# Kernel tuning notes

Hardware: AMD Instinct MI355X
Metric: run time of the kernel (lower is better)

The kernel has to match this reference:

```python
import jax, jax.numpy as jnp
import numpy as np
from jax import lax

B, T, N = 32, 48, 360   # batch, time steps, ROIs
H = 100                 # LSTM hidden (self.L)
D = 64                  # attention hidden (self.D)
K = 1                   # attention heads (self.K)
NUM_CLASS = 2


def setup_inputs() -> dict:
    key = jax.random.key(0)
    ks = jax.random.split(key, 14)
    s = 0.02
    return {
        "x": jax.random.normal(ks[0], (B, T, N, N), dtype=jnp.float32),
        # GCN: Linear(ROInum, 1) applied to (x @ I)
        "w_gcn": jax.random.normal(ks[1], (N,), dtype=jnp.float32) * s,
        "b_gcn": jnp.zeros((), dtype=jnp.float32),
        # LSTM (pytorch layout: [4H, in] with gate order i,f,g,o)
        "W_ih": jax.random.normal(ks[2], (4 * H, N), dtype=jnp.float32) * s,
        "W_hh": jax.random.normal(ks[3], (4 * H, H), dtype=jnp.float32) * s,
        "b_ih": jnp.zeros((4 * H,), dtype=jnp.float32),
        "b_hh": jnp.zeros((4 * H,), dtype=jnp.float32),
        # attention MLP: Linear(L,D) -> tanh -> Linear(D,K)
        "wa1": jax.random.normal(ks[4], (D, H), dtype=jnp.float32) * s,
        "ba1": jnp.zeros((D,), dtype=jnp.float32),
        "wa2": jax.random.normal(ks[5], (K, D), dtype=jnp.float32) * s,
        "ba2": jnp.zeros((K,), dtype=jnp.float32),
        # classifier: Linear(L*K, num_class) -> softmax (dropout inactive at eval)
        "wc": jax.random.normal(ks[6], (NUM_CLASS, H * K), dtype=jnp.float32) * s,
        "bc": jnp.zeros((NUM_CLASS,), dtype=jnp.float32),
    }


def _lstm(seq, W_ih, W_HH, b):
    # seq: [B, T, N] -> hidden states [B, T, H]
    def step(carry, xt):
        h, c = carry
        gates = xt @ W_ih.T + h @ W_HH.T + b  # [B, 4H]
        i, f, g, o = jnp.split(gates, 4, axis=-1)
        i, f, o = jax.nn.sigmoid(i), jax.nn.sigmoid(f), jax.nn.sigmoid(o)
        c = f * c + i * jnp.tanh(g)
        h = o * jnp.tanh(c)
        return (h, c), h

    h0 = jnp.zeros((seq.shape[0], H), seq.dtype)
    c0 = jnp.zeros((seq.shape[0], H), seq.dtype)
    _, hs = lax.scan(step, (h0, c0), jnp.swapaxes(seq, 0, 1))
    return jnp.swapaxes(hs, 0, 1)


def reference(x, w_gcn, b_gcn, W_ih, W_hh, b_ih, b_hh, wa1, ba1, wa2, ba2, wc, bc):
    # GCN per (sample, timestep): h = relu(Linear(x @ I)) == relu(x @ w + b)
    # batched over B and T in one einsum (eliminates the python loops).
    gout = jax.nn.relu(jnp.einsum("btnm,m->btn", x, w_gcn) + b_gcn)  # [B,T,N]

    out = _lstm(gout, W_ih, W_hh, b_ih + b_hh)  # [B,T,H]

    # MIL attention: A = Linear(tanh(Linear(out)))
    A = jnp.tanh(jnp.einsum("bth,dh->btd", out, wa1) + ba1)
    A = jnp.einsum("btd,kd->btk", A, wa2) + ba2          # [B,T,K]
    A = jnp.swapaxes(A, 2, 1)                             # [B,K,T]
    Att = A
    A = jax.nn.softmax(A, axis=2)
    M = jnp.einsum("bkt,bth->bkh", A, out).reshape(x.shape[0], H * K)

    Y_prob = jax.nn.softmax(M @ wc.T + bc, axis=1)  # dropout is identity at eval
    return (Y_prob, Att)
```

## Files before the change

kernel.cpp:

```cpp
#include <hip/hip_runtime.h>
#include <math.h>

#define BB 32
#define TT 48
#define NN 360
#define HH 100
#define DD 64
#define NC 2
#define G4 400

typedef float vf4 __attribute__((ext_vector_type(4)));

__device__ __forceinline__ float sigmoid_fast(float x) {
    return 1.f / (1.f + __expf(-x));
}
__device__ __forceinline__ float tanh_fast(float x) {
    float ax = fabsf(x);
    float e = __expf(-2.f * ax);
    float t = (1.f - e) / (1.f + e);
    return copysignf(t, x);
}
__device__ __forceinline__ float bcast_lane(float v, int l) {
    return __int_as_float(__builtin_amdgcn_readlane(__float_as_int(v), l));
}
__device__ __forceinline__ vf4 ntload4(const float* p) {
    return __builtin_nontemporal_load((const vf4*)p);
}
__device__ __forceinline__ float dotslot(vf4 a, vf4 w) {
    return fmaf(a.w, w.w, fmaf(a.z, w.z, fmaf(a.y, w.y, a.x * w.x)));
}

#define DPP_ADD(x, ctrl, rmask) \
    x += __int_as_float(__builtin_amdgcn_update_dpp(0, __float_as_int(x), ctrl, rmask, 0xf, true));
#define WAVE_RED(p) \
    DPP_ADD(p, 0x111, 0xf) DPP_ADD(p, 0x112, 0xf) DPP_ADD(p, 0x114, 0xf) DPP_ADD(p, 0x118, 0xf) \
    DPP_ADD(p, 0x142, 0xa) DPP_ADD(p, 0x143, 0xc)

#define RG 8
#define NGROUPS (BB*TT*NN/RG)
#define GF4 (RG*NN/4)
#define LOADG(S, gidx) do { if ((gidx) < NGROUPS) { \
    const float* gb_ = x + (size_t)(gidx) * (RG * NN); \
    S##0  = ntload4(gb_ + 0*256  + 4*lane); \
    S##1  = ntload4(gb_ + 1*256  + 4*lane); \
    S##2  = ntload4(gb_ + 2*256  + 4*lane); \
    S##3  = ntload4(gb_ + 3*256  + 4*lane); \
    S##4  = ntload4(gb_ + 4*256  + 4*lane); \
    S##5  = ntload4(gb_ + 5*256  + 4*lane); \
    S##6  = ntload4(gb_ + 6*256  + 4*lane); \
    S##7  = ntload4(gb_ + 7*256  + 4*lane); \
    S##8  = ntload4(gb_ + 8*256  + 4*lane); \
    S##9  = ntload4(gb_ + 9*256  + 4*lane); \
    S##10 = ntload4(gb_ + 10*256 + 4*lane); \
    if (lane < 16) S##11 = ntload4(gb_ + 11*256 + 4*lane); \
} } while (0)
#define WRITELDS(S) do { \
    buf[0*64  + lane] = S##0; \
    buf[1*64  + lane] = S##1; \
    buf[2*64  + lane] = S##2; \
    buf[3*64  + lane] = S##3; \
    buf[4*64  + lane] = S##4; \
    buf[5*64  + lane] = S##5; \
    buf[6*64  + lane] = S##6; \
    buf[7*64  + lane] = S##7; \
    buf[8*64  + lane] = S##8; \
    buf[9*64  + lane] = S##9; \
    buf[10*64 + lane] = S##10; \
    if (lane < 16) buf[11*64 + lane] = S##11; \
} while (0)
#define COMPUTE_STORE(gcur) do { \
    float s_[RG]; \
    _Pragma("unroll") \
    for (int r = 0; r < RG; ++r) { \
        vf4 a_ = buf[r*90 + lane]; \
        float p_ = dotslot(a_, wa); \
        if (lane < 26) { vf4 a2_ = buf[r*90 + 64 + lane]; p_ += dotslot(a2_, wb); } \
        WAVE_RED(p_) \
        s_[r] = p_; \
    } \
    if (lane == 63) { \
        float4 o0_, o1_; \
        o0_.x = fmaxf(s_[0] + b, 0.f); o0_.y = fmaxf(s_[1] + b, 0.f); \
        o0_.z = fmaxf(s_[2] + b, 0.f); o0_.w = fmaxf(s_[3] + b, 0.f); \
        o1_.x = fmaxf(s_[4] + b, 0.f); o1_.y = fmaxf(s_[5] + b, 0.f); \
        o1_.z = fmaxf(s_[6] + b, 0.f); o1_.w = fmaxf(s_[7] + b, 0.f); \
        ((float4*)gout)[2*(gcur)]     = o0_; \
        ((float4*)gout)[2*(gcur) + 1] = o1_; \
    } \
} while (0)

__global__ __launch_bounds__(256) void gcn_kernel(const float* __restrict__ x,
                                                  const float* __restrict__ w,
                                                  const float* __restrict__ bptr,
                                                  float* __restrict__ gout) {
    __shared__ __align__(16) vf4 sbuf[4][GF4];
    int tid = threadIdx.x;
    int lane = tid & 63;
    int wv = tid >> 6;
    vf4* buf = sbuf[wv];
    vf4 wa = *(const vf4*)(w + 4*lane);
    vf4 wb;
    if (lane < 26) wb = *(const vf4*)(w + 4*(64 + lane));
    else { wb.x = 0.f; wb.y = 0.f; wb.z = 0.f; wb.w = 0.f; }
    float b = bptr[0];
    const int gstride = gridDim.x * 4;
    int g = blockIdx.x * 4 + wv;
    vf4 sa0, sa1, sa2, sa3, sa4, sa5, sa6, sa7, sa8, sa9, sa10, sa11;
    vf4 sb0, sb1, sb2, sb3, sb4, sb5, sb6, sb7, sb8, sb9, sb10, sb11;
    LOADG(sa, g);
    LOADG(sb, g + gstride);
    for (int g2 = g; g2 < NGROUPS; ) {
        __builtin_amdgcn_sched_barrier(0);
        WRITELDS(sa);
        LOADG(sa, g2 + 2*gstride);
        COMPUTE_STORE(g2);
        g2 += gstride;
        if (g2 >= NGROUPS) break;
        __builtin_amdgcn_sched_barrier(0);
        WRITELDS(sb);
        LOADG(sb, g2 + 2*gstride);
        COMPUTE_STORE(g2);
        g2 += gstride;
    }
}

__global__ void transpose_wih(const float* __restrict__ Wih, float* __restrict__ Wt2) {
    int idx = blockIdx.x * blockDim.x + threadIdx.x;
    if (idx < NN * G4) {
        int j = idx / NN, n = idx % NN;
        Wt2[n * G4 + 2 * (j % 200) + (j / 200)] = Wih[idx];
    }
}

__global__ __launch_bounds__(256) void xproj_kernel(const float* __restrict__ gout,
                                                    const float* __restrict__ Wt2,
                                                    const float* __restrict__ b_ih,
                                                    const float* __restrict__ b_hh,
                                                    float* __restrict__ xproj) {
    int tid = threadIdx.x;
    if (tid >= 200) return;
    int r0 = blockIdx.x * 4;
    float acc00 = 0.f, acc01 = 0.f, acc10 = 0.f, acc11 = 0.f;
    float acc20 = 0.f, acc21 = 0.f, acc30 = 0.f, acc31 = 0.f;
    const float* g0p = gout + (size_t)(r0 + 0) * NN;
    const float* g1p = gout + (size_t)(r0 + 1) * NN;
    const float* g2p = gout + (size_t)(r0 + 2) * NN;
    const float* g3p = gout + (size_t)(r0 + 3) * NN;
    const float* wp = Wt2 + 2 * tid;
    for (int n = 0; n < NN; n += 4) {
        float4 g0 = *(const float4*)(g0p + n);
        float4 g1 = *(const float4*)(g1p + n);
        float4 g2 = *(const float4*)(g2p + n);
        float4 g3 = *(const float4*)(g3p + n);
        float2 wA = *(const float2*)(wp + (n + 0) * G4);
        float2 wB = *(const float2*)(wp + (n + 1) * G4);
        float2 wC = *(const float2*)(wp + (n + 2) * G4);
        float2 wD = *(const float2*)(wp + (n + 3) * G4);
        acc00 += g0.x*wA.x + g0.y*wB.x + g0.z*wC.x + g0.w*wD.x;
        acc01 += g0.x*wA.y + g0.y*wB.y + g0.z*wC.y + g0.w*wD.y;
        acc10 += g1.x*wA.x + g1.y*wB.x + g1.z*wC.x + g1.w*wD.x;
        acc11 += g1.x*wA.y + g1.y*wB.y + g1.z*wC.y + g1.w*wD.y;
        acc20 += g2.x*wA.x + g2.y*wB.x + g2.z*wC.x + g2.w*wD.x;
        acc21 += g2.x*wA.y + g2.y*wB.y + g2.z*wC.y + g2.w*wD.y;
        acc30 += g3.x*wA.x + g3.y*wB.x + g3.z*wC.x + g3.w*wD.x;
        acc31 += g3.x*wA.y + g3.y*wB.y + g3.z*wC.y + g3.w*wD.y;
    }
    float bias0 = b_ih[tid] + b_hh[tid];
    float bias1 = b_ih[tid + 200] + b_hh[tid + 200];
    xproj[(size_t)(r0 + 0) * G4 + tid]       = acc00 + bias0;
    xproj[(size_t)(r0 + 0) * G4 + tid + 200] = acc01 + bias1;
    xproj[(size_t)(r0 + 1) * G4 + tid]       = acc10 + bias0;
    xproj[(size_t)(r0 + 1) * G4 + tid + 200] = acc11 + bias1;
    xproj[(size_t)(r0 + 2) * G4 + tid]       = acc20 + bias0;
    xproj[(size_t)(r0 + 2) * G4 + tid + 200] = acc21 + bias1;
    xproj[(size_t)(r0 + 3) * G4 + tid]       = acc30 + bias0;
    xproj[(size_t)(r0 + 3) * G4 + tid + 200] = acc31 + bias1;
}

__global__ __launch_bounds__(448) void lstm_attn_kernel(const float* __restrict__ xproj,
                                                        const float* __restrict__ Whh,
                                                        const float* __restrict__ wa1,
                                                        const float* __restrict__ ba1,
                                                        const float* __restrict__ wa2,
                                                        const float* __restrict__ ba2,
                                                        const float* __restrict__ wc,
                                                        const float* __restrict__ bc,
                                                        float* __restrict__ out) {
    __shared__ __align__(16) float ho[TT * HH];
    __shared__ __align__(16) float h_lds[128];
    __shared__ float gates[G4];
    __shared__ float sc[TT];
    __shared__ float p[TT];
    __shared__ float M[HH];
    int b = blockIdx.x;
    int tid = threadIdx.x;
    int lane = tid & 63;
    float wr[HH];
    if (tid < G4) {
        #pragma unroll
        for (int k = 0; k < HH; k++) wr[k] = Whh[tid * HH + k];
    }
    float c = 0.f;
    if (tid < 128) h_lds[tid] = 0.f;
    float xp = (tid < G4) ? xproj[(size_t)(b * TT) * G4 + tid] : 0.f;
    __syncthreads();
    for (int t = 0; t < TT; t++) {
        float xp_next = (tid < G4 && t + 1 < TT)
                      ? xproj[(size_t)(b * TT + t + 1) * G4 + tid] : 0.f;
        float ha = h_lds[lane];
        float hb = h_lds[64 + lane];
        if (tid < G4) {
            float s0 = 0.f, s1 = 0.f, s2 = 0.f, s3 = 0.f;
            #pragma unroll
            for (int k = 0; k < 64; k += 4) {
                s0 += bcast_lane(ha, k+0) * wr[k+0];
                s1 += bcast_lane(ha, k+1) * wr[k+1];
                s2 += bcast_lane(ha, k+2) * wr[k+2];
                s3 += bcast_lane(ha, k+3) * wr[k+3];
            }
            #pragma unroll
            for (int k = 64; k < 100; k += 4) {
                s0 += bcast_lane(hb, k-64) * wr[k+0];
                s1 += bcast_lane(hb, k-63) * wr[k+1];
                s2 += bcast_lane(hb, k-62) * wr[k+2];
                s3 += bcast_lane(hb, k-61) * wr[k+3];
            }
            gates[tid] = xp + (s0 + s1) + (s2 + s3);
        }
        __syncthreads();
        if (tid < HH) {
            float ig = sigmoid_fast(gates[tid]);
            float fg = sigmoid_fast(gates[tid + HH]);
            float gg = tanh_fast(gates[tid + 2*HH]);
            float og = sigmoid_fast(gates[tid + 3*HH]);
            c = fg * c + ig * gg;
            float hh = og * tanh_fast(c);
            h_lds[tid] = hh;
            ho[t * HH + tid] = hh;
        }
        xp = xp_next;
        __syncthreads();
    }
    int wave = tid >> 6;
    for (int t = wave; t < TT; t += 7) {
        float a = 0.f;
        if (lane < DD) {
            float s = ba1[lane];
            #pragma unroll
            for (int h2 = 0; h2 < HH; h2 += 4) {
                float4 h4v = *(const float4*)&ho[t*HH + h2];
                s += wa1[lane*HH + h2+0]*h4v.x + wa1[lane*HH + h2+1]*h4v.y
                   + wa1[lane*HH + h2+2]*h4v.z + wa1[lane*HH + h2+3]*h4v.w;
            }
            a = tanh_fast(s) * wa2[lane];
        }
        #pragma unroll
        for (int off = 32; off; off >>= 1) a += __shfl_down(a, off, 64);
        if (lane == 0) sc[t] = a + ba2[0];
    }
    __syncthreads();
    if (tid < 64) {
        float v = (lane < TT) ? sc[lane] : -1e30f;
        if (lane < TT) out[BB*NC + b*TT + lane] = v;
        float m = v;
        #pragma unroll
        for (int off = 32; off; off >>= 1) m = fmaxf(m, __shfl_xor(m, off, 64));
        float e = (lane < TT) ? __expf(v - m) : 0.f;
        float s = e;
        #pragma unroll
        for (int off = 32; off; off >>= 1) s += __shfl_xor(s, off, 64);
        if (lane < TT) p[lane] = e / s;
    }
    __syncthreads();
    if (tid < HH) {
        float m = 0.f;
        #pragma unroll
        for (int t = 0; t < TT; t++) m += p[t] * ho[t*HH + tid];
        M[tid] = m;
    }
    __syncthreads();
    if (tid == 0) {
        float l0 = bc[0], l1 = bc[1];
        for (int h2 = 0; h2 < HH; h2++) { l0 += M[h2]*wc[h2]; l1 += M[h2]*wc[HH + h2]; }
        float mx = fmaxf(l0, l1);
        float e0 = __expf(l0 - mx), e1 = __expf(l1 - mx);
        float s = e0 + e1;
        out[b*NC + 0] = e0 / s;
        out[b*NC + 1] = e1 / s;
    }
}

extern "C" void kernel_launch(void* const* d_in, const int* in_sizes, int n_in,
                              void* d_out, int out_size, void* d_ws, size_t ws_size,
                              hipStream_t stream) {
    const float* x     = (const float*)d_in[0];
    const float* w_gcn = (const float*)d_in[1];
    const float* b_gcn = (const float*)d_in[2];
    const float* W_ih  = (const float*)d_in[3];
    const float* W_hh  = (const float*)d_in[4];
    const float* b_ih  = (const float*)d_in[5];
    const float* b_hh  = (const float*)d_in[6];
    const float* wa1   = (const float*)d_in[7];
    const float* ba1   = (const float*)d_in[8];
    const float* wa2   = (const float*)d_in[9];
    const float* ba2   = (const float*)d_in[10];
    const float* wc    = (const float*)d_in[11];
    const float* bc    = (const float*)d_in[12];
    float* out = (float*)d_out;
    float* ws  = (float*)d_ws;

    float* gout  = ws;
    float* Wt2   = gout + 552960;
    float* xproj = Wt2 + 144000;

    transpose_wih<<<(NN*G4 + 255)/256, 256, 0, stream>>>(W_ih, Wt2);
    gcn_kernel<<<768, 256, 0, stream>>>(x, w_gcn, b_gcn, gout);
    xproj_kernel<<<384, 256, 0, stream>>>(gout, Wt2, b_ih, b_hh, xproj);
    lstm_attn_kernel<<<BB, 448, 0, stream>>>(xproj, W_hh, wa1, ba1, wa2, ba2, wc, bc, out);
}
```

Measured before the change: 213.8 us.

## Interleave LSTM gate rows per quad and exchange gates via DPP

```diff
diff --git a/kernel.cpp b/kernel.cpp
--- a/kernel.cpp
+++ b/kernel.cpp
@@ -22,6 +22,10 @@
 }
 __device__ __forceinline__ float bcast_lane(float v, int l) {
     return __int_as_float(__builtin_amdgcn_readlane(__float_as_int(v), l));
+}
+template <int CTRL>
+__device__ __forceinline__ float quad_bcast(float v) {
+    return __int_as_float(__builtin_amdgcn_update_dpp(0, __float_as_int(v), CTRL, 0xf, 0xf, true));
 }
 __device__ __forceinline__ vf4 ntload4(const float* p) {
     return __builtin_nontemporal_load((const vf4*)p);
@@ -124,57 +128,48 @@
     }
 }
 
-__global__ void transpose_wih(const float* __restrict__ Wih, float* __restrict__ Wt2) {
+__global__ void transpose_wih(const float* __restrict__ Wih, float* __restrict__ Wt) {
     int idx = blockIdx.x * blockDim.x + threadIdx.x;
     if (idx < NN * G4) {
         int j = idx / NN, n = idx % NN;
-        Wt2[n * G4 + 2 * (j % 200) + (j / 200)] = Wih[idx];
-    }
-}
-
-__global__ __launch_bounds__(256) void xproj_kernel(const float* __restrict__ gout,
-                                                    const float* __restrict__ Wt2,
+        Wt[n * G4 + j] = Wih[idx];
+    }
+}
+
+__global__ __launch_bounds__(448) void xproj_kernel(const float* __restrict__ gout,
+                                                    const float* __restrict__ Wt,
                                                     const float* __restrict__ b_ih,
                                                     const float* __restrict__ b_hh,
                                                     float* __restrict__ xproj) {
     int tid = threadIdx.x;
-    if (tid >= 200) return;
+    if (tid >= G4) return;
     int r0 = blockIdx.x * 4;
-    float acc00 = 0.f, acc01 = 0.f, acc10 = 0.f, acc11 = 0.f;
-    float acc20 = 0.f, acc21 = 0.f, acc30 = 0.f, acc31 = 0.f;
+    float a0 = 0.f, a1 = 0.f, a2 = 0.f, a3 = 0.f;
     const float* g0p = gout + (size_t)(r0 + 0) * NN;
     const float* g1p = gout + (size_t)(r0 + 1) * NN;
     const float* g2p = gout + (size_t)(r0 + 2) * NN;
     const float* g3p = gout + (size_t)(r0 + 3) * NN;
-    const float* wp = Wt2 + 2 * tid;
+    const float* wp = Wt + tid;
     for (int n = 0; n < NN; n += 4) {
+        float w0 = wp[(n+0)*G4];
+        float w1 = wp[(n+1)*G4];
+        float w2 = wp[(n+2)*G4];
+        float w3 = wp[(n+3)*G4];
         float4 g0 = *(const float4*)(g0p + n);
         float4 g1 = *(const float4*)(g1p + n);
         float4 g2 = *(const float4*)(g2p + n);
         float4 g3 = *(const float4*)(g3p + n);
-        float2 wA = *(const float2*)(wp + (n + 0) * G4);
-        float2 wB = *(const float2*)(wp + (n + 1) * G4);
-        float2 wC = *(const float2*)(wp + (n + 2) * G4);
-        float2 wD = *(const float2*)(wp + (n + 3) * G4);
-        acc00 += g0.x*wA.x + g0.y*wB.x + g0.z*wC.x + g0.w*wD.x;
-        acc01 += g0.x*wA.y + g0.y*wB.y + g0.z*wC.y + g0.w*wD.y;
-        acc10 += g1.x*wA.x + g1.y*wB.x + g1.z*wC.x + g1.w*wD.x;
-        acc11 += g1.x*wA.y + g1.y*wB.y + g1.z*wC.y + g1.w*wD.y;
-        acc20 += g2.x*wA.x + g2.y*wB.x + g2.z*wC.x + g2.w*wD.x;
-        acc21 += g2.x*wA.y + g2.y*wB.y + g2.z*wC.y + g2.w*wD.y;
-        acc30 += g3.x*wA.x + g3.y*wB.x + g3.z*wC.x + g3.w*wD.x;
-        acc31 += g3.x*wA.y + g3.y*wB.y + g3.z*wC.y + g3.w*wD.y;
-    }
-    float bias0 = b_ih[tid] + b_hh[tid];
-    float bias1 = b_ih[tid + 200] + b_hh[tid + 200];
-    xproj[(size_t)(r0 + 0) * G4 + tid]       = acc00 + bias0;
-    xproj[(size_t)(r0 + 0) * G4 + tid + 200] = acc01 + bias1;
-    xproj[(size_t)(r0 + 1) * G4 + tid]       = acc10 + bias0;
-    xproj[(size_t)(r0 + 1) * G4 + tid + 200] = acc11 + bias1;
-    xproj[(size_t)(r0 + 2) * G4 + tid]       = acc20 + bias0;
-    xproj[(size_t)(r0 + 2) * G4 + tid + 200] = acc21 + bias1;
-    xproj[(size_t)(r0 + 3) * G4 + tid]       = acc30 + bias0;
-    xproj[(size_t)(r0 + 3) * G4 + tid + 200] = acc31 + bias1;
+        a0 += g0.x*w0 + g0.y*w1 + g0.z*w2 + g0.w*w3;
+        a1 += g1.x*w0 + g1.y*w1 + g1.z*w2 + g1.w*w3;
+        a2 += g2.x*w0 + g2.y*w1 + g2.z*w2 + g2.w*w3;
+        a3 += g3.x*w0 + g3.y*w1 + g3.z*w2 + g3.w*w3;
+    }
+    float bias = b_ih[tid] + b_hh[tid];
+    int pj = 4 * (tid % HH) + (tid / HH);
+    xproj[(size_t)(r0 + 0) * G4 + pj] = a0 + bias;
+    xproj[(size_t)(r0 + 1) * G4 + pj] = a1 + bias;
+    xproj[(size_t)(r0 + 2) * G4 + pj] = a2 + bias;
+    xproj[(size_t)(r0 + 3) * G4 + pj] = a3 + bias;
 }
 
 __global__ __launch_bounds__(448) void lstm_attn_kernel(const float* __restrict__ xproj,
@@ -187,28 +182,32 @@
                                                         const float* __restrict__ bc,
                                                         float* __restrict__ out) {
     __shared__ __align__(16) float ho[TT * HH];
-    __shared__ __align__(16) float h_lds[128];
-    __shared__ float gates[G4];
+    __shared__ __align__(16) float hbuf[2][128];
     __shared__ float sc[TT];
     __shared__ float p[TT];
     __shared__ float M[HH];
     int b = blockIdx.x;
     int tid = threadIdx.x;
     int lane = tid & 63;
+    int g = tid & 3;
+    int j = tid >> 2;
     float wr[HH];
     if (tid < G4) {
-        #pragma unroll
-        for (int k = 0; k < HH; k++) wr[k] = Whh[tid * HH + k];
+        int row = g * HH + j;
+        #pragma unroll
+        for (int k = 0; k < HH; k++) wr[k] = Whh[row * HH + k];
     }
     float c = 0.f;
-    if (tid < 128) h_lds[tid] = 0.f;
+    if (tid < 128) { hbuf[0][tid] = 0.f; hbuf[1][tid] = 0.f; }
     float xp = (tid < G4) ? xproj[(size_t)(b * TT) * G4 + tid] : 0.f;
     __syncthreads();
     for (int t = 0; t < TT; t++) {
+        int pcur = t & 1;
         float xp_next = (tid < G4 && t + 1 < TT)
                       ? xproj[(size_t)(b * TT + t + 1) * G4 + tid] : 0.f;
-        float ha = h_lds[lane];
-        float hb = h_lds[64 + lane];
+        float ha = hbuf[pcur][lane];
+        float hb = hbuf[pcur][64 + lane];
+        float v = xp;
         if (tid < G4) {
             float s0 = 0.f, s1 = 0.f, s2 = 0.f, s3 = 0.f;
             #pragma unroll
@@ -225,18 +224,21 @@
                 s2 += bcast_lane(hb, k-62) * wr[k+2];
                 s3 += bcast_lane(hb, k-61) * wr[k+3];
             }
-            gates[tid] = xp + (s0 + s1) + (s2 + s3);
+            v = xp + (s0 + s1) + (s2 + s3);
         }
-        __syncthreads();
-        if (tid < HH) {
-            float ig = sigmoid_fast(gates[tid]);
-            float fg = sigmoid_fast(gates[tid + HH]);
-            float gg = tanh_fast(gates[tid + 2*HH]);
-            float og = sigmoid_fast(gates[tid + 3*HH]);
+        float vi = quad_bcast<0x00>(v);
+        float vf = quad_bcast<0x55>(v);
+        float vg = quad_bcast<0xAA>(v);
+        float vo = quad_bcast<0xFF>(v);
+        if (tid < G4 && g == 0) {
+            float ig = sigmoid_fast(vi);
+            float fg = sigmoid_fast(vf);
+            float gg = tanh_fast(vg);
+            float og = sigmoid_fast(vo);
             c = fg * c + ig * gg;
             float hh = og * tanh_fast(c);
-            h_lds[tid] = hh;
-            ho[t * HH + tid] = hh;
+            hbuf[1 - pcur][j] = hh;
+            ho[t * HH + j] = hh;
         }
         xp = xp_next;
         __syncthreads();
@@ -310,11 +312,11 @@
     float* ws  = (float*)d_ws;
 
     float* gout  = ws;
-    float* Wt2   = gout + 552960;
-    float* xproj = Wt2 + 144000;
-
-    transpose_wih<<<(NN*G4 + 255)/256, 256, 0, stream>>>(W_ih, Wt2);
+    float* Wt    = gout + 552960;
+    float* xproj = Wt + 144000;
+
+    transpose_wih<<<(NN*G4 + 255)/256, 256, 0, stream>>>(W_ih, Wt);
     gcn_kernel<<<768, 256, 0, stream>>>(x, w_gcn, b_gcn, gout);
-    xproj_kernel<<<384, 256, 0, stream>>>(gout, Wt2, b_ih, b_hh, xproj);
+    xproj_kernel<<<384, 448, 0, stream>>>(gout, Wt, b_ih, b_hh, xproj);
     lstm_attn_kernel<<<BB, 448, 0, stream>>>(xproj, W_hh, wa1, ba1, wa2, ba2, wc, bc, out);
 }
```

New measurement: 213.0 us. No clear change (-0.4%).
